# Optimization experiments

Measured on AMD Instinct MI355X. Metric: run time of the kernel, lower is better.

The kernel has to match this reference:

```python
import jax, jax.numpy as jnp
import numpy as np

# NF4 codebook (QLoRA): 16 quantile values of a standard normal, normalized to [-1, 1]
NF4_TABLE = jnp.array([
    -1.0, -0.6961928009986877, -0.5250730514526367, -0.39491748809814453,
    -0.28444138169288635, -0.18477343022823334, -0.09105003625154495, 0.0,
    0.07958029955625534, 0.16093020141124725, 0.24611230194568634,
    0.33791524171829224, 0.44070982933044434, 0.5626170039176941,
    0.7229568362236328, 1.0], dtype=jnp.float32)

IN_DIM = 4096
OUT_DIM = 4096
RANK = 16
ALPHA = 32.0
BLOCK = 64  # NF4 quantization block size along the flattened weight


def setup_inputs() -> dict:
    key = jax.random.key(0)
    k1, k2, k3, k4, k5 = jax.random.split(key, 5)
    x = jax.random.normal(k1, (4, 2048, IN_DIM), dtype=jnp.float32)
    # 4-bit codes into NF4_TABLE, stored unpacked as int32
    w_codes = jax.random.randint(k2, (OUT_DIM, IN_DIM), 0, 16, dtype=jnp.int32)
    # per-block absmax scales (positive)
    w_scales = jax.random.uniform(k3, (OUT_DIM, IN_DIM // BLOCK), dtype=jnp.float32) * 0.02 + 1e-3
    # lora_a: kaiming-uniform-ish scale; lora_b: nonzero for testability (original inits to zeros)
    lora_a = jax.random.normal(k4, (RANK, IN_DIM), dtype=jnp.float32) * (1.0 / np.sqrt(IN_DIM))
    lora_b = jax.random.normal(k5, (OUT_DIM, RANK), dtype=jnp.float32) * 0.01
    return {"x": x, "w_codes": w_codes, "w_scales": w_scales, "lora_a": lora_a, "lora_b": lora_b}


def _dequant_nf4(w_codes, w_scales):
    # codes [O, I] -> dequantized weight [O, I]
    w = NF4_TABLE[w_codes]                                   # [O, I]
    w = w.reshape(OUT_DIM, IN_DIM // BLOCK, BLOCK) * w_scales[:, :, None]
    return w.reshape(OUT_DIM, IN_DIM)


def reference(x, w_codes, w_scales, lora_a, lora_b):
    # base: frozen NF4 linear (dequantize then matmul), no bias
    w = _dequant_nf4(w_codes, w_scales)                      # [O, I]
    base = jnp.einsum('bsi,oi->bso', x, w)                   # [B, S, O]
    # LoRA path: dropout p=0.0 -> identity; scale alpha / rank
    ax = jnp.einsum('bsi,ri->bsr', x, lora_a)                # [B, S, r]
    lora = jnp.einsum('bsr,or->bso', ax, lora_b)             # [B, S, O]
    return base + (ALPHA / RANK) * lora
```

## Files before the change

kernel.cpp:

```cpp
#include <hip/hip_runtime.h>
#include <hip/hip_bf16.h>


#define IN_DIM  4096
#define OUT_DIM 4096
#define RANK    16
#define M_TOK   8192
#define LORA_SCALE 2.0f

typedef __bf16 bf16_t;
typedef bf16_t bf16x8 __attribute__((ext_vector_type(8)));
typedef float  f32x4  __attribute__((ext_vector_type(4)));

__device__ __constant__ float NF4_TAB[16] = {
    -1.0f, -0.6961928009986877f, -0.5250730514526367f, -0.39491748809814453f,
    -0.28444138169288635f, -0.18477343022823334f, -0.09105003625154495f, 0.0f,
    0.07958029955625534f, 0.16093020141124725f, 0.24611230194568634f,
    0.33791524171829224f, 0.44070982933044434f, 0.5626170039176941f,
    0.7229568362236328f, 1.0f};

__global__ __launch_bounds__(256) void prep_all(
    const float* __restrict__ x,
    const int* __restrict__ codes, const float* __restrict__ scales,
    const float* __restrict__ la, const float* __restrict__ lb,
    bf16_t* __restrict__ W, bf16_t* __restrict__ xb)
{
    const int tid = threadIdx.x;
    if (blockIdx.x < 1024) {
        __shared__ float nf4s[16];
        __shared__ float lbs[4][16];
        const int o0 = blockIdx.x * 4;
        if (tid < 64) lbs[tid >> 4][tid & 15] = lb[(o0 + (tid >> 4)) * RANK + (tid & 15)] * LORA_SCALE;
        else if (tid < 80) nf4s[tid - 64] = NF4_TAB[tid - 64];
        __syncthreads();

        #pragma unroll
        for (int it = 0; it < 2; ++it) {
            const int i0 = (it * 256 + tid) * 8;
            float w[4][8];
            #pragma unroll
            for (int oo = 0; oo < 4; ++oo) {
                const size_t base = (size_t)(o0 + oo) * IN_DIM + i0;
                int4 c0 = *(const int4*)(codes + base);
                int4 c1 = *(const int4*)(codes + base + 4);
                const float sc = scales[(o0 + oo) * (IN_DIM / 64) + (i0 >> 6)];
                w[oo][0] = nf4s[c0.x] * sc; w[oo][1] = nf4s[c0.y] * sc;
                w[oo][2] = nf4s[c0.z] * sc; w[oo][3] = nf4s[c0.w] * sc;
                w[oo][4] = nf4s[c1.x] * sc; w[oo][5] = nf4s[c1.y] * sc;
                w[oo][6] = nf4s[c1.z] * sc; w[oo][7] = nf4s[c1.w] * sc;
            }
            #pragma unroll
            for (int r = 0; r < RANK; ++r) {
                float4 a0 = *(const float4*)(la + r * IN_DIM + i0);
                float4 a1 = *(const float4*)(la + r * IN_DIM + i0 + 4);
                #pragma unroll
                for (int oo = 0; oo < 4; ++oo) {
                    const float b = lbs[oo][r];
                    w[oo][0] += b * a0.x; w[oo][1] += b * a0.y;
                    w[oo][2] += b * a0.z; w[oo][3] += b * a0.w;
                    w[oo][4] += b * a1.x; w[oo][5] += b * a1.y;
                    w[oo][6] += b * a1.z; w[oo][7] += b * a1.w;
                }
            }
            #pragma unroll
            for (int oo = 0; oo < 4; ++oo) {
                bf16x8 v;
                #pragma unroll
                for (int j = 0; j < 8; ++j) v[j] = (bf16_t)w[oo][j];
                *(bf16x8*)(W + (size_t)(o0 + oo) * IN_DIM + i0) = v;
            }
        }
    } else {
        const int bid = blockIdx.x - 1024;
        const int n8 = (M_TOK * IN_DIM) / 8;
        const int stride = 2048 * 256;
        for (int i = bid * 256 + tid; i < n8; i += stride) {
            const size_t e = (size_t)i * 8;
            float4 a = *(const float4*)(x + e);
            float4 b = *(const float4*)(x + e + 4);
            bf16x8 v;
            v[0] = (bf16_t)a.x; v[1] = (bf16_t)a.y; v[2] = (bf16_t)a.z; v[3] = (bf16_t)a.w;
            v[4] = (bf16_t)b.x; v[5] = (bf16_t)b.y; v[6] = (bf16_t)b.z; v[7] = (bf16_t)b.w;
            *(bf16x8*)(xb + e) = v;
        }
    }
}

__global__ __launch_bounds__(512, 2) void gemm_bt(
    const bf16_t* __restrict__ A, const bf16_t* __restrict__ B,
    float* __restrict__ C)
{
    __shared__ __align__(128) char lds[131072];

    const int tid  = threadIdx.x;
    const int wave = tid >> 6;
    const int lane = tid & 63;

    const int flat = blockIdx.y * gridDim.x + blockIdx.x;
    const int swz  = (flat & 7) * 64 + (flat >> 3);
    const int bx = swz & 15;
    const int by = swz >> 4;
    const int m0 = by * 256;
    const int n0 = bx * 256;

    const int wr = wave >> 2;
    const int wc = wave & 3;

    f32x4 acc[8][4];
    #pragma unroll
    for (int i = 0; i < 8; ++i)
        #pragma unroll
        for (int j = 0; j < 4; ++j) acc[i][j] = (f32x4)0.0f;

    const int frow = lane & 15;
    const int fch  = lane >> 4;
    const int fxor = (fch ^ ((frow >> 1) & 3)) << 4;
    const int aoff = (wr * 128 + frow) * 64 + fxor;
    const int boff = (wc * 64  + frow) * 64 + fxor;

    const int d0 = tid * 16, d1 = 8192 + tid * 16;
    const int sr0 = d0 >> 6, sr1 = d1 >> 6;
    const int sg0 = ((d0 >> 4) & 3) ^ ((sr0 >> 1) & 3);
    const int sg1 = ((d1 >> 4) & 3) ^ ((sr1 >> 1) & 3);
    const char* gA = (const char*)A;
    const char* gB = (const char*)B;

    bf16x8 fAe[8], fAo[8], fBe[2], fBo[2];

#define RD_A2(FA, SL, KH, J0) do {                                             \
    const char* b_ = lds + (SL) * 65536 + (KH) * 16384;                        \
    FA[(J0)]     = *(const bf16x8*)(b_ + aoff + (J0) * 1024);                  \
    FA[(J0) + 1] = *(const bf16x8*)(b_ + aoff + ((J0) + 1) * 1024);            \
} while (0)

#define RD_B(FB, SL, KH, NH) do {                                              \
    const char* b_ = lds + (SL) * 65536 + 32768 + (KH) * 16384;                \
    FB[0] = *(const bf16x8*)(b_ + boff + (NH) * 2048);                         \
    FB[1] = *(const bf16x8*)(b_ + boff + (NH) * 2048 + 1024);                  \
} while (0)

#define STG1(OPI, KH_, SL, T) do {                                             \
    const char* g_  = (OPI) ? gB : gA;                                         \
    const int   r0_ = (OPI) ? n0 : m0;                                         \
    const size_t ko_ = (size_t)(T) * 128 + (KH_) * 64;                         \
    const char* s0_ = g_ + (size_t)(r0_ + sr0) * 8192 + ko_ + (sg0 << 4);      \
    const char* s1_ = g_ + (size_t)(r0_ + sr1) * 8192 + ko_ + (sg1 << 4);      \
    char* db_ = lds + (SL) * 65536 + (OPI) * 32768 + (KH_) * 16384 + wave * 1024; \
    __builtin_amdgcn_global_load_lds(                                          \
        (const __attribute__((address_space(1))) void*)s0_,                    \
        (__attribute__((address_space(3))) void*)db_, 16, 0, 0);               \
    __builtin_amdgcn_global_load_lds(                                          \
        (const __attribute__((address_space(1))) void*)s1_,                    \
        (__attribute__((address_space(3))) void*)(db_ + 8192), 16, 0, 0);      \
} while (0)

#define MM4(FA, F0, FB, BI, NH) do {                                           \
    _Pragma("unroll")                                                          \
    for (int f_ = 0; f_ < 4; ++f_)                                             \
        acc[(F0) + f_][(NH) * 2 + (BI)] =                                      \
            __builtin_amdgcn_mfma_f32_16x16x32_bf16(                           \
                FA[(F0) + f_], FB[BI], acc[(F0) + f_][(NH) * 2 + (BI)], 0, 0, 0); \
} while (0)

#define REGION(FA, FAN, RSL, RKH, A_OP, A_KH, A_SL, A_T, B_OP, B_KH, B_SL, B_T) do { \
    STG1(A_OP, A_KH, A_SL, A_T);                                               \
    __builtin_amdgcn_s_setprio(1);                                             \
    MM4(FA, 0, fBe, 0, 0);                                                     \
    MM4(FA, 4, fBe, 0, 0);                                                     \
    RD_A2(FAN, RSL, RKH, 0);                                                   \
    MM4(FA, 0, fBe, 1, 0);                                                     \
    MM4(FA, 4, fBe, 1, 0);                                                     \
    RD_B(fBe, RSL, RKH, 0);                                                    \
    STG1(B_OP, B_KH, B_SL, B_T);                                               \
    MM4(FA, 0, fBo, 0, 1);                                                     \
    RD_A2(FAN, RSL, RKH, 2);                                                   \
    MM4(FA, 4, fBo, 0, 1);                                                     \
    RD_A2(FAN, RSL, RKH, 4);                                                   \
    MM4(FA, 0, fBo, 1, 1);                                                     \
    RD_A2(FAN, RSL, RKH, 6);                                                   \
    MM4(FA, 4, fBo, 1, 1);                                                     \
    RD_B(fBo, RSL, RKH, 1);                                                    \
    __builtin_amdgcn_s_setprio(0);                                             \
    asm volatile("s_waitcnt vmcnt(4)" ::: "memory");                           \
    __builtin_amdgcn_s_barrier();                                              \
} while (0)

    STG1(0, 0, 0, 0); STG1(1, 0, 0, 0); STG1(0, 1, 0, 0); STG1(1, 1, 0, 0);
    STG1(0, 0, 1, 1); STG1(1, 0, 1, 1);
    asm volatile("s_waitcnt vmcnt(4)" ::: "memory");
    __builtin_amdgcn_s_barrier();
    RD_A2(fAe, 0, 0, 0); RD_A2(fAe, 0, 0, 2);
    RD_A2(fAe, 0, 0, 4); RD_A2(fAe, 0, 0, 6);
    RD_B(fBe, 0, 0, 0);  RD_B(fBo, 0, 0, 1);

    for (int i = 0; i < 32; ++i) {
        const int tY  = 2 * i + 1;
        const int tS0 = (2 * i + 2) & 63;
        const int tS1 = (2 * i + 3) & 63;
        REGION(fAe, fAo, 0, 1,  0, 1, 1, tY,   1, 1, 1, tY);
        REGION(fAo, fAe, 1, 0,  0, 0, 0, tS0,  1, 0, 0, tS0);
        REGION(fAe, fAo, 1, 1,  0, 1, 0, tS0,  1, 1, 0, tS0);
        REGION(fAo, fAe, 0, 0,  0, 0, 1, tS1,  1, 0, 1, tS1);
    }

    const int crow = (lane >> 4) * 4;
    const int ccol = lane & 15;
    #pragma unroll
    for (int i = 0; i < 8; ++i) {
        #pragma unroll
        for (int j = 0; j < 4; ++j) {
            const int mb = m0 + wr * 128 + i * 16 + crow;
            const int nb = n0 + wc * 64 + j * 16 + ccol;
            #pragma unroll
            for (int r = 0; r < 4; ++r)
                C[(size_t)(mb + r) * OUT_DIM + nb] = acc[i][j][r];
        }
    }
#undef RD_A2
#undef RD_B
#undef STG1
#undef MM4
#undef REGION
}

extern "C" void kernel_launch(void* const* d_in, const int* in_sizes, int n_in,
                              void* d_out, int out_size, void* d_ws, size_t ws_size,
                              hipStream_t stream) {
    const float* x      = (const float*)d_in[0];
    const int*   codes  = (const int*)d_in[1];
    const float* scales = (const float*)d_in[2];
    const float* la     = (const float*)d_in[3];
    const float* lb     = (const float*)d_in[4];
    float* out = (float*)d_out;

    bf16_t* W  = (bf16_t*)d_ws;
    bf16_t* xb = (bf16_t*)((char*)d_ws + (size_t)OUT_DIM * IN_DIM * 2);

    prep_all<<<1024 + 2048, 256, 0, stream>>>(x, codes, scales, la, lb, W, xb);

    dim3 grid(OUT_DIM / 256, M_TOK / 256);
    gemm_bt<<<grid, 512, 0, stream>>>(xb, W, out);
}
```

Before: 286.9 us.

## Shrink GEMM tile to 128x256 with triple-buffered K=32 LDS pipeline

The bf16 GEMM block tile drops from 256x256 to 128x256 and the K step from 64 to 32. The two-slot, half-K-split LDS schedule with register double-buffered fragments is replaced by a simpler three-slot ring buffer, with one barrier per step and all fragments loaded before the MFMAs. LDS use falls from 128KB to 72KB and launch bounds ask for 4 blocks per CU to raise occupancy. In exchange, each block reuses less data, so global/L2 traffic per FLOP rises, barriers become more frequent, and LDS reads no longer overlap with MFMA inside a step.

```diff
diff --git a/kernel.cpp b/kernel.cpp
--- a/kernel.cpp
+++ b/kernel.cpp
@@ -86,141 +86,113 @@
     }
 }
 
-__global__ __launch_bounds__(512, 2) void gemm_bt(
+__global__ __launch_bounds__(512, 4) void gemm_bt(
     const bf16_t* __restrict__ A, const bf16_t* __restrict__ B,
     float* __restrict__ C)
 {
-    __shared__ __align__(128) char lds[131072];
+    __shared__ __align__(128) char lds[3][24576];
 
     const int tid  = threadIdx.x;
     const int wave = tid >> 6;
     const int lane = tid & 63;
 
     const int flat = blockIdx.y * gridDim.x + blockIdx.x;
-    const int swz  = (flat & 7) * 64 + (flat >> 3);
+    const int swz  = (flat & 7) * 128 + (flat >> 3);
     const int bx = swz & 15;
     const int by = swz >> 4;
-    const int m0 = by * 256;
+    const int m0 = by * 128;
     const int n0 = bx * 256;
 
     const int wr = wave >> 2;
     const int wc = wave & 3;
 
-    f32x4 acc[8][4];
+    f32x4 acc[4][4];
     #pragma unroll
-    for (int i = 0; i < 8; ++i)
+    for (int i = 0; i < 4; ++i)
         #pragma unroll
         for (int j = 0; j < 4; ++j) acc[i][j] = (f32x4)0.0f;
 
     const int frow = lane & 15;
     const int fch  = lane >> 4;
     const int fxor = (fch ^ ((frow >> 1) & 3)) << 4;
-    const int aoff = (wr * 128 + frow) * 64 + fxor;
-    const int boff = (wc * 64  + frow) * 64 + fxor;
-
-    const int d0 = tid * 16, d1 = 8192 + tid * 16;
-    const int sr0 = d0 >> 6, sr1 = d1 >> 6;
-    const int sg0 = ((d0 >> 4) & 3) ^ ((sr0 >> 1) & 3);
-    const int sg1 = ((d1 >> 4) & 3) ^ ((sr1 >> 1) & 3);
+    const int aoff = (wr * 64 + frow) * 64 + fxor;
+    const int boff = (wc * 64 + frow) * 64 + fxor;
+
+    const int srow = tid >> 2;
+    const int sg   = ((tid & 3) ^ ((srow >> 1) & 3)) << 4;
+    const int sgB2 = ((tid & 3) ^ (((srow + 128) >> 1) & 3)) << 4;
     const char* gA = (const char*)A;
     const char* gB = (const char*)B;
 
-    bf16x8 fAe[8], fAo[8], fBe[2], fBo[2];
-
-#define RD_A2(FA, SL, KH, J0) do {                                             \
-    const char* b_ = lds + (SL) * 65536 + (KH) * 16384;                        \
-    FA[(J0)]     = *(const bf16x8*)(b_ + aoff + (J0) * 1024);                  \
-    FA[(J0) + 1] = *(const bf16x8*)(b_ + aoff + ((J0) + 1) * 1024);            \
-} while (0)
-
-#define RD_B(FB, SL, KH, NH) do {                                              \
-    const char* b_ = lds + (SL) * 65536 + 32768 + (KH) * 16384;                \
-    FB[0] = *(const bf16x8*)(b_ + boff + (NH) * 2048);                         \
-    FB[1] = *(const bf16x8*)(b_ + boff + (NH) * 2048 + 1024);                  \
-} while (0)
-
-#define STG1(OPI, KH_, SL, T) do {                                             \
-    const char* g_  = (OPI) ? gB : gA;                                         \
-    const int   r0_ = (OPI) ? n0 : m0;                                         \
-    const size_t ko_ = (size_t)(T) * 128 + (KH_) * 64;                         \
-    const char* s0_ = g_ + (size_t)(r0_ + sr0) * 8192 + ko_ + (sg0 << 4);      \
-    const char* s1_ = g_ + (size_t)(r0_ + sr1) * 8192 + ko_ + (sg1 << 4);      \
-    char* db_ = lds + (SL) * 65536 + (OPI) * 32768 + (KH_) * 16384 + wave * 1024; \
+#define STG(T, SL) do {                                                        \
+    const size_t ko_ = (size_t)(T) * 64;                                       \
+    const char* sa_ = gA + (size_t)(m0 + srow) * 8192 + ko_ + sg;              \
+    const char* sb0_ = gB + (size_t)(n0 + srow) * 8192 + ko_ + sg;             \
+    const char* sb1_ = gB + (size_t)(n0 + 128 + srow) * 8192 + ko_ + sgB2;     \
+    char* da_ = &lds[SL][0] + wave * 1024;                                     \
+    char* db_ = &lds[SL][8192] + wave * 1024;                                  \
     __builtin_amdgcn_global_load_lds(                                          \
-        (const __attribute__((address_space(1))) void*)s0_,                    \
+        (const __attribute__((address_space(1))) void*)sa_,                    \
+        (__attribute__((address_space(3))) void*)da_, 16, 0, 0);               \
+    __builtin_amdgcn_global_load_lds(                                          \
+        (const __attribute__((address_space(1))) void*)sb0_,                   \
         (__attribute__((address_space(3))) void*)db_, 16, 0, 0);               \
     __builtin_amdgcn_global_load_lds(                                          \
-        (const __attribute__((address_space(1))) void*)s1_,                    \
+        (const __attribute__((address_space(1))) void*)sb1_,                   \
         (__attribute__((address_space(3))) void*)(db_ + 8192), 16, 0, 0);      \
 } while (0)
 
-#define MM4(FA, F0, FB, BI, NH) do {                                           \
+#define STEP(T, SL, STSL, DO_STG, VMN) do {                                    \
+    asm volatile("s_waitcnt vmcnt(" #VMN ")" ::: "memory");                    \
+    __builtin_amdgcn_s_barrier();                                              \
+    bf16x8 fA[4], fB[4];                                                       \
+    {                                                                          \
+        const char* b_ = &lds[SL][0];                                          \
+        _Pragma("unroll")                                                      \
+        for (int f_ = 0; f_ < 4; ++f_)                                         \
+            fA[f_] = *(const bf16x8*)(b_ + aoff + f_ * 1024);                  \
+        _Pragma("unroll")                                                      \
+        for (int j_ = 0; j_ < 4; ++j_)                                         \
+            fB[j_] = *(const bf16x8*)(b_ + 8192 + boff + j_ * 1024);           \
+    }                                                                          \
+    if (DO_STG) STG((T) + 2, STSL);                                            \
+    __builtin_amdgcn_s_setprio(1);                                             \
     _Pragma("unroll")                                                          \
-    for (int f_ = 0; f_ < 4; ++f_)                                             \
-        acc[(F0) + f_][(NH) * 2 + (BI)] =                                      \
-            __builtin_amdgcn_mfma_f32_16x16x32_bf16(                           \
-                FA[(F0) + f_], FB[BI], acc[(F0) + f_][(NH) * 2 + (BI)], 0, 0, 0); \
+    for (int i_ = 0; i_ < 4; ++i_)                                             \
+        _Pragma("unroll")                                                      \
+        for (int j_ = 0; j_ < 4; ++j_)                                         \
+            acc[i_][j_] = __builtin_amdgcn_mfma_f32_16x16x32_bf16(             \
+                fA[i_], fB[j_], acc[i_][j_], 0, 0, 0);                         \
+    __builtin_amdgcn_s_setprio(0);                                             \
 } while (0)
 
-#define REGION(FA, FAN, RSL, RKH, A_OP, A_KH, A_SL, A_T, B_OP, B_KH, B_SL, B_T) do { \
-    STG1(A_OP, A_KH, A_SL, A_T);                                               \
-    __builtin_amdgcn_s_setprio(1);                                             \
-    MM4(FA, 0, fBe, 0, 0);                                                     \
-    MM4(FA, 4, fBe, 0, 0);                                                     \
-    RD_A2(FAN, RSL, RKH, 0);                                                   \
-    MM4(FA, 0, fBe, 1, 0);                                                     \
-    MM4(FA, 4, fBe, 1, 0);                                                     \
-    RD_B(fBe, RSL, RKH, 0);                                                    \
-    STG1(B_OP, B_KH, B_SL, B_T);                                               \
-    MM4(FA, 0, fBo, 0, 1);                                                     \
-    RD_A2(FAN, RSL, RKH, 2);                                                   \
-    MM4(FA, 4, fBo, 0, 1);                                                     \
-    RD_A2(FAN, RSL, RKH, 4);                                                   \
-    MM4(FA, 0, fBo, 1, 1);                                                     \
-    RD_A2(FAN, RSL, RKH, 6);                                                   \
-    MM4(FA, 4, fBo, 1, 1);                                                     \
-    RD_B(fBo, RSL, RKH, 1);                                                    \
-    __builtin_amdgcn_s_setprio(0);                                             \
-    asm volatile("s_waitcnt vmcnt(4)" ::: "memory");                           \
-    __builtin_amdgcn_s_barrier();                                              \
-} while (0)
-
-    STG1(0, 0, 0, 0); STG1(1, 0, 0, 0); STG1(0, 1, 0, 0); STG1(1, 1, 0, 0);
-    STG1(0, 0, 1, 1); STG1(1, 0, 1, 1);
-    asm volatile("s_waitcnt vmcnt(4)" ::: "memory");
-    __builtin_amdgcn_s_barrier();
-    RD_A2(fAe, 0, 0, 0); RD_A2(fAe, 0, 0, 2);
-    RD_A2(fAe, 0, 0, 4); RD_A2(fAe, 0, 0, 6);
-    RD_B(fBe, 0, 0, 0);  RD_B(fBo, 0, 0, 1);
-
-    for (int i = 0; i < 32; ++i) {
-        const int tY  = 2 * i + 1;
-        const int tS0 = (2 * i + 2) & 63;
-        const int tS1 = (2 * i + 3) & 63;
-        REGION(fAe, fAo, 0, 1,  0, 1, 1, tY,   1, 1, 1, tY);
-        REGION(fAo, fAe, 1, 0,  0, 0, 0, tS0,  1, 0, 0, tS0);
-        REGION(fAe, fAo, 1, 1,  0, 1, 0, tS0,  1, 1, 0, tS0);
-        REGION(fAo, fAe, 0, 0,  0, 0, 1, tS1,  1, 0, 1, tS1);
+    STG(0, 0);
+    STG(1, 1);
+
+    for (int j = 0; j < 42; ++j) {
+        const int t = 3 * j;
+        STEP(t,     0, 2, 1, 3);
+        STEP(t + 1, 1, 0, 1, 3);
+        STEP(t + 2, 2, 1, 1, 3);
     }
+    STEP(126, 0, 0, 0, 3);
+    STEP(127, 1, 0, 0, 0);
 
     const int crow = (lane >> 4) * 4;
     const int ccol = lane & 15;
     #pragma unroll
-    for (int i = 0; i < 8; ++i) {
+    for (int i = 0; i < 4; ++i) {
         #pragma unroll
         for (int j = 0; j < 4; ++j) {
-            const int mb = m0 + wr * 128 + i * 16 + crow;
+            const int mb = m0 + wr * 64 + i * 16 + crow;
             const int nb = n0 + wc * 64 + j * 16 + ccol;
             #pragma unroll
             for (int r = 0; r < 4; ++r)
                 C[(size_t)(mb + r) * OUT_DIM + nb] = acc[i][j][r];
         }
     }
-#undef RD_A2
-#undef RD_B
-#undef STG1
-#undef MM4
-#undef REGION
+#undef STG
+#undef STEP
 }
 
 extern "C" void kernel_launch(void* const* d_in, const int* in_sizes, int n_in,
@@ -238,6 +210,6 @@
 
     prep_all<<<1024 + 2048, 256, 0, stream>>>(x, codes, scales, la, lb, W, xb);
 
-    dim3 grid(OUT_DIM / 256, M_TOK / 256);
+    dim3 grid(OUT_DIM / 256, M_TOK / 128);
     gemm_bt<<<grid, 512, 0, stream>>>(xb, W, out);
 }
```

Result: slower. 333.0 us (+16.0%).
